# Optimization experiments

Hardware: AMD Instinct MI355X
Metric: run time of the kernel (lower is better)

The kernel has to match this reference:

```python
import jax, jax.numpy as jnp
import numpy as np

N = 100000          # nodes
E = 3200000         # edges per order (avg degree 32)
F_IN = 512          # num_features
HID = 128           # args.hidden
ORDER = 2
K = 10              # propagation hops
ALPHA = 0.1
C = 10              # num_classes


def setup_inputs() -> dict:
    key = jax.random.key(0)
    ks = jax.random.split(key, 10)
    x = jax.random.normal(ks[0], (N, F_IN), dtype=jnp.float32)
    edge_index1 = jax.random.randint(ks[1], (2, E), 0, N, dtype=jnp.int32)
    edge_weight1 = jax.random.uniform(ks[2], (E,), dtype=jnp.float32) / 32.0  # ~row-normalized
    edge_index2 = jax.random.randint(ks[3], (2, E), 0, N, dtype=jnp.int32)
    edge_weight2 = jax.random.uniform(ks[4], (E,), dtype=jnp.float32) / 32.0
    W_in = jax.random.normal(ks[5], (ORDER, F_IN, HID), dtype=jnp.float32) * 0.05
    b_in = jnp.zeros((ORDER, HID), dtype=jnp.float32)
    # GPR filter weights: fW[k] = alpha*(1-alpha)^k, fW[K] = (1-alpha)^K
    k_arr = np.arange(K + 1, dtype=np.float32)
    fw = ALPHA * (1.0 - ALPHA) ** k_arr
    fw[-1] = (1.0 - ALPHA) ** K
    fW = jnp.broadcast_to(jnp.asarray(fw), (ORDER, K + 1)).astype(jnp.float32)
    W_out = jax.random.normal(ks[6], (HID * ORDER, C), dtype=jnp.float32) * 0.05
    b_out = jnp.zeros((C,), dtype=jnp.float32)
    return {"x": x, "edge_index1": edge_index1, "edge_weight1": edge_weight1,
            "edge_index2": edge_index2, "edge_weight2": edge_weight2,
            "W_in": W_in, "b_in": b_in, "fW": fW, "W_out": W_out, "b_out": b_out}


def _spmm(edge_index, edge_weight, h, n):
    # y[row] += w * h[col]  (COO SpMM with add-aggregation)
    row, col = edge_index[0], edge_index[1]
    return jax.ops.segment_sum(edge_weight[:, None] * h[col], row, num_segments=n)


def reference(x, edge_index1, edge_weight1, edge_index2, edge_weight2,
              W_in, b_in, fW, W_out, b_out):
    n = x.shape[0]
    branches = [(edge_index1, edge_weight1), (edge_index2, edge_weight2)]
    outs = []
    for i, (ei, ew) in enumerate(branches):
        h = x @ W_in[i] + b_in[i]                 # [N, HID]  (dropout inactive in eval)
        hidden = h * fW[i, 0]
        for k in range(K):                        # K-hop GPR-weighted propagation
            h = _spmm(ei, ew, h, n)
            hidden = hidden + fW[i, k + 1] * h
        outs.append(hidden)
    z = jnp.concatenate(outs, axis=1) @ W_out + b_out   # [N, C]
    return jax.nn.log_softmax(z, axis=1)
```

## Files before the change

kernel.cpp:

```cpp
#include <hip/hip_runtime.h>

#define F_IN 512
#define HID 128
#define KHOPS 10
#define COUT 10

typedef unsigned int uint;
typedef unsigned short ushort;
typedef float f32x4 __attribute__((ext_vector_type(4)));
typedef short bf16x8 __attribute__((ext_vector_type(8)));
typedef int v16i __attribute__((ext_vector_type(16)));

__device__ __forceinline__ uint f2bf1(float f) {
    uint u = __float_as_uint(f);
    return (u + 0x7fffu + ((u >> 16) & 1u)) >> 16;
}
__device__ __forceinline__ uint packbf(float a, float b) {
    return f2bf1(a) | (f2bf1(b) << 16);
}
__device__ __forceinline__ float bflo(uint u) { return __uint_as_float(u << 16); }
__device__ __forceinline__ float bfhi(uint u) { return __uint_as_float(u & 0xffff0000u); }

__global__ __launch_bounds__(256) void wprep_kernel(
    const float* __restrict__ Win, ushort* __restrict__ Wsw)
{
    const int t = blockIdx.x * blockDim.x + threadIdx.x;
    if (t >= 2 * 16 * 8 * 64) return;
    const int l = t & 63;
    const int c = (t >> 6) & 7;
    const int s = (t >> 9) & 15;
    const int br = t >> 13;
    const int col = c * 16 + (l & 15);
    const int k0 = s * 32 + (l >> 4) * 8;
    const float* W = Win + (size_t)br * F_IN * HID;
    uint o0 = packbf(W[(size_t)(k0 + 0) * HID + col], W[(size_t)(k0 + 1) * HID + col]);
    uint o1 = packbf(W[(size_t)(k0 + 2) * HID + col], W[(size_t)(k0 + 3) * HID + col]);
    uint o2 = packbf(W[(size_t)(k0 + 4) * HID + col], W[(size_t)(k0 + 5) * HID + col]);
    uint o3 = packbf(W[(size_t)(k0 + 6) * HID + col], W[(size_t)(k0 + 7) * HID + col]);
    *(uint4*)(Wsw + (size_t)t * 8) = make_uint4(o0, o1, o2, o3);
}

__global__ __launch_bounds__(256) void gemm_mfma_kernel(
    const float* __restrict__ x, const ushort* __restrict__ Wsw,
    const float* __restrict__ bin, uint* __restrict__ h1, uint* __restrict__ h2, int n)
{
    const int br = blockIdx.y;
    const uint4* Wb = (const uint4*)(Wsw + (size_t)br * 16 * 8 * 64 * 8);
    const float* bias = bin + br * HID;
    uint* h = br ? h2 : h1;

    const int w = threadIdx.x >> 6;
    const int lane = threadIdx.x & 63;
    const int r16 = lane & 15;
    const int kg = lane >> 4;

    const int rowbase = blockIdx.x * 128 + w * 32;

    f32x4 acc[2][8];
#pragma unroll
    for (int f = 0; f < 2; ++f)
#pragma unroll
        for (int c = 0; c < 8; ++c) acc[f][c] = (f32x4)0.f;

    int rA0 = rowbase + r16;      if (rA0 > n - 1) rA0 = n - 1;
    int rA1 = rowbase + 16 + r16; if (rA1 > n - 1) rA1 = n - 1;
    const float* xp0 = x + (size_t)rA0 * F_IN + kg * 8;
    const float* xp1 = x + (size_t)rA1 * F_IN + kg * 8;

    for (int s = 0; s < 16; ++s) {
        const float4 a0lo = *(const float4*)(xp0 + s * 32);
        const float4 a0hi = *(const float4*)(xp0 + s * 32 + 4);
        const float4 a1lo = *(const float4*)(xp1 + s * 32);
        const float4 a1hi = *(const float4*)(xp1 + s * 32 + 4);
        union { uint4 u; bf16x8 v; } af0, af1;
        af0.u = make_uint4(packbf(a0lo.x, a0lo.y), packbf(a0lo.z, a0lo.w),
                           packbf(a0hi.x, a0hi.y), packbf(a0hi.z, a0hi.w));
        af1.u = make_uint4(packbf(a1lo.x, a1lo.y), packbf(a1lo.z, a1lo.w),
                           packbf(a1hi.x, a1hi.y), packbf(a1hi.z, a1hi.w));
        const uint4* wq = Wb + (size_t)(s * 8) * 64 + lane;
#pragma unroll
        for (int c = 0; c < 8; ++c) {
            union { uint4 u; bf16x8 v; } bfr;
            bfr.u = wq[c * 64];
            acc[0][c] = __builtin_amdgcn_mfma_f32_16x16x32_bf16(af0.v, bfr.v, acc[0][c], 0, 0, 0);
            acc[1][c] = __builtin_amdgcn_mfma_f32_16x16x32_bf16(af1.v, bfr.v, acc[1][c], 0, 0, 0);
        }
    }

    float bv[8];
#pragma unroll
    for (int c = 0; c < 8; ++c) bv[c] = bias[c * 16 + r16];

#pragma unroll
    for (int f = 0; f < 2; ++f)
#pragma unroll
        for (int c = 0; c < 8; ++c)
#pragma unroll
            for (int i = 0; i < 4; ++i) {
                const float v = acc[f][c][i] + bv[c];
                const float o = __shfl_xor(v, 1);
                const int row = rowbase + f * 16 + kg * 4 + i;
                if (!(lane & 1) && row < n)
                    h[(size_t)row * 64 + c * 8 + (r16 >> 1)] = packbf(v, o);
            }
}


__global__ void bhist_kernel(const int* __restrict__ r1, int E1,
                             const int* __restrict__ r2, int E2,
                             int* __restrict__ bcnt, int nb)
{
    extern __shared__ int sh[];
    const int br = blockIdx.y;
    const int* rows = br ? r2 : r1;
    const int E = br ? E2 : E1;
    int* bc = bcnt + (size_t)br * nb;
    for (int i = threadIdx.x; i < nb; i += blockDim.x) sh[i] = 0;
    __syncthreads();
    for (int i = blockIdx.x * blockDim.x + threadIdx.x; i < E; i += gridDim.x * blockDim.x)
        atomicAdd(&sh[rows[i] >> 6], 1);
    __syncthreads();
    for (int i = threadIdx.x; i < nb; i += blockDim.x)
        if (sh[i]) atomicAdd(&bc[i], sh[i]);
}

__global__ __launch_bounds__(256) void bscan_kernel(
    const int* __restrict__ bcnt, int* __restrict__ bbase, int* __restrict__ bcur,
    int* __restrict__ rowp1, int* __restrict__ rowp2,
    int nb, int n, int E1, int E2)
{
    __shared__ int ssum[256];
    const int br = blockIdx.y;
    const int* bc = bcnt + (size_t)br * nb;
    int* bb = bbase + (size_t)br * (nb + 1);
    int* cur = bcur + (size_t)br * nb;
    int* rowp = br ? rowp2 : rowp1;
    const int E = br ? E2 : E1;
    const int t = threadIdx.x;
    const int chunk = (nb + 255) / 256;
    const int start = t * chunk;
    const int end = (start + chunk < nb) ? start + chunk : nb;
    int sum = 0;
    for (int i = start; i < end; ++i) sum += bc[i];
    ssum[t] = sum;
    __syncthreads();
    if (t == 0) {
        int run = 0;
        for (int i = 0; i < 256; ++i) { int v = ssum[i]; ssum[i] = run; run += v; }
        bb[nb] = E;
        rowp[n] = E;
    }
    __syncthreads();
    int run = ssum[t];
    for (int i = start; i < end; ++i) {
        bb[i] = run; cur[i] = run; run += bc[i];
    }
}

#define SCAT_BLOCKS 256
__global__ __launch_bounds__(256) void bscat_kernel(
    const int* __restrict__ r1, const int* __restrict__ c1, const float* __restrict__ w1, int E1,
    const int* __restrict__ r2, const int* __restrict__ c2, const float* __restrict__ w2, int E2,
    int* __restrict__ bcur, int2* __restrict__ t1, int2* __restrict__ t2, int nb)
{
    extern __shared__ int sh[];
    int* lh = sh;
    int* lbase = sh + nb;
    const int br = blockIdx.y;
    const int* rows = br ? r2 : r1;
    const int* cols = br ? c2 : c1;
    const float* w  = br ? w2 : w1;
    const int E = br ? E2 : E1;
    int* cur = bcur + (size_t)br * nb;
    int2* tcw = br ? t2 : t1;
    const int t = threadIdx.x;

    for (int i = t; i < nb; i += 256) lh[i] = 0;
    __syncthreads();

    const int per = (E + SCAT_BLOCKS - 1) / SCAT_BLOCKS;
    const int c0 = blockIdx.x * per;
    const int cend = (c0 + per < E) ? c0 + per : E;

    for (int i = c0 + t; i < cend; i += 256)
        atomicAdd(&lh[rows[i] >> 6], 1);
    __syncthreads();
    for (int b = t; b < nb; b += 256) {
        int c = lh[b];
        lbase[b] = c ? atomicAdd(&cur[b], c) : 0;
        lh[b] = 0;
    }
    __syncthreads();
    for (int i = c0 + t; i < cend; i += 256) {
        int r = rows[i];
        int b = r >> 6;
        int p = atomicAdd(&lh[b], 1);
        uint lo = ((uint)cols[i] << 8) | (uint)(r & 63);
        tcw[lbase[b] + p] = make_int2((int)lo, __float_as_int(w[i]));
    }
}

__global__ __launch_bounds__(256) void bsort_kernel(
    const int* __restrict__ bbase,
    const int2* __restrict__ t1, const int2* __restrict__ t2,
    int* __restrict__ rowp1, int* __restrict__ rowp2,
    int2* __restrict__ cw1, int2* __restrict__ cw2, int nb, int n)
{
    __shared__ int cnt[64], soff[64], pos[64];
    const int br = blockIdx.y;
    const int* bb = bbase + (size_t)br * (nb + 1);
    const int2* tcw = br ? t2 : t1;
    int* rowp = br ? rowp2 : rowp1;
    int2* cw = br ? cw2 : cw1;
    const int b = blockIdx.x;
    const int t = threadIdx.x;
    const int base = bb[b];
    const int m = bb[b + 1] - base;
    if (t < 64) cnt[t] = 0;
    __syncthreads();
    for (int i = t; i < m; i += 256) atomicAdd(&cnt[(uint)tcw[base + i].x & 63], 1);
    __syncthreads();
    if (t == 0) {
        int run = 0;
#pragma unroll
        for (int r = 0; r < 64; ++r) { soff[r] = run; run += cnt[r]; }
    }
    __syncthreads();
    if (t < 64) {
        pos[t] = soff[t];
        int g = b * 64 + t;
        if (g < n) rowp[g] = base + soff[t];
    }
    __syncthreads();
    for (int i = t; i < m; i += 256) {
        int2 e = tcw[base + i];
        int r = (uint)e.x & 63;
        int p = atomicAdd(&pos[r], 1);
        cw[base + p] = make_int2((int)((uint)e.x & 0xFFFFFF00u), e.y);
    }
}

struct BrArgs {
    const int* rowp;
    const int2* cw;
    const uint* hin;
    uint* hout;
    const float* Wo;
};

__global__ __launch_bounds__(256) void spmm2_kernel(
    BrArgs A, BrArgs B, const float* __restrict__ fW, int k,
    float* __restrict__ z2, int storeH, int n)
{
    const int bid = blockIdx.x;
    const int br = bid & 1;
    const int wid = (bid >> 1) * 4 + (threadIdx.x >> 6);
    if (wid >= n) return;
    const int*   rowp = br ? B.rowp : A.rowp;
    const int2*  cw   = br ? B.cw   : A.cw;
    const uint*  hin  = br ? B.hin  : A.hin;
    uint*        hout = br ? B.hout : A.hout;
    const float* Wo   = br ? B.Wo   : A.Wo;
    const int lane = threadIdx.x & 63;
    const uint laneB = (uint)lane * 4u;
    const char* hbase = (const char*)hin;

    float w0[COUT], w1[COUT];
    const float* wp = Wo + (size_t)(lane * 2) * COUT;
#pragma unroll
    for (int c = 0; c < COUT; ++c) { w0[c] = wp[c]; w1[c] = wp[COUT + c]; }

    int s = rowp[wid];
    int e = rowp[wid + 1];
    s = __builtin_amdgcn_readfirstlane(s);
    e = __builtin_amdgcn_readfirstlane(e);

    float2 acc = make_float2(0.f, 0.f);
    int i = s;

    while (e - i >= 16) {
        v16i e0v, e1v;
        asm volatile("s_load_dwordx16 %0, %2, 0x0\n\t"
                     "s_load_dwordx16 %1, %2, 0x40\n\t"
                     "s_waitcnt lgkmcnt(0)"
                     : "=s"(e0v), "=s"(e1v) : "s"(cw + i));
#pragma unroll
        for (int j = 0; j < 8; ++j) {
            const uint boff = (uint)e0v[2 * j];
            const float q = __int_as_float(e0v[2 * j + 1]);
            const uint g = *(const uint*)(hbase + (size_t)boff + laneB);
            acc.x = fmaf(q, bflo(g), acc.x);
            acc.y = fmaf(q, bfhi(g), acc.y);
        }
#pragma unroll
        for (int j = 0; j < 8; ++j) {
            const uint boff = (uint)e1v[2 * j];
            const float q = __int_as_float(e1v[2 * j + 1]);
            const uint g = *(const uint*)(hbase + (size_t)boff + laneB);
            acc.x = fmaf(q, bflo(g), acc.x);
            acc.y = fmaf(q, bfhi(g), acc.y);
        }
        i += 16;
    }
    const int rem = e - i;
    if (rem > 0) {
        v16i e0v, e1v;
        asm volatile("s_load_dwordx16 %0, %2, 0x0\n\t"
                     "s_load_dwordx16 %1, %2, 0x40\n\t"
                     "s_waitcnt lgkmcnt(0)"
                     : "=s"(e0v), "=s"(e1v) : "s"(cw + i));
#pragma unroll
        for (int j = 0; j < 16; ++j) {
            uint boff = (uint)((j < 8) ? e0v[2 * j] : e1v[2 * (j - 8)]);
            float q = __int_as_float((j < 8) ? e0v[2 * j + 1] : e1v[2 * (j - 8) + 1]);
            if (j >= rem) { boff = 0u; q = 0.f; }
            const uint g = *(const uint*)(hbase + (size_t)boff + laneB);
            acc.x = fmaf(q, bflo(g), acc.x);
            acc.y = fmaf(q, bfhi(g), acc.y);
        }
    }

    if (storeH)
        hout[(size_t)wid * 64 + lane] = packbf(acc.x, acc.y);

    const float fw = fW[br * (KHOPS + 1) + k + 1];
    float zadd = 0.f;
#pragma unroll
    for (int c = 0; c < COUT; ++c) {
        float pp = fmaf(acc.x, w0[c], acc.y * w1[c]);
#pragma unroll
        for (int off = 32; off; off >>= 1) pp += __shfl_xor(pp, off);
        if (lane == c) zadd = pp;
    }
    if (lane < COUT) {
        const size_t o = (size_t)wid * (2 * COUT) + br * COUT + lane;
        z2[o] += fw * zadd;
    }
}

__global__ __launch_bounds__(256) void zacc2_kernel(
    const uint* __restrict__ h1, const uint* __restrict__ h2,
    const float* __restrict__ Wout, const float* __restrict__ fW,
    float* __restrict__ z2, int n)
{
    const int wid = (blockIdx.x * blockDim.x + threadIdx.x) >> 6;
    if (wid >= n) return;
    const int lane = threadIdx.x & 63;
    const uint u1 = h1[(size_t)wid * 64 + lane];
    const uint u2 = h2[(size_t)wid * 64 + lane];
    const float a1 = bflo(u1), b1v = bfhi(u1);
    const float a2 = bflo(u2), b2v = bfhi(u2);
    const float* wp1 = Wout + (size_t)(lane * 2) * COUT;
    const float* wp2 = Wout + (size_t)HID * COUT + (size_t)(lane * 2) * COUT;
    float zv1 = 0.f, zv2 = 0.f;
#pragma unroll
    for (int c = 0; c < COUT; ++c) {
        float p1 = fmaf(a1, wp1[c], b1v * wp1[COUT + c]);
        float p2 = fmaf(a2, wp2[c], b2v * wp2[COUT + c]);
#pragma unroll
        for (int off = 32; off; off >>= 1) { p1 += __shfl_xor(p1, off); p2 += __shfl_xor(p2, off); }
        if (lane == c) { zv1 = p1; zv2 = p2; }
    }
    if (lane < COUT) {
        z2[(size_t)wid * (2 * COUT) + lane]        = fW[0] * zv1;
        z2[(size_t)wid * (2 * COUT) + COUT + lane] = fW[KHOPS + 1] * zv2;
    }
}

__global__ void logsm_kernel(const float* __restrict__ z2, const float* __restrict__ bout,
                             float* __restrict__ out, int n)
{
    const int r = blockIdx.x * blockDim.x + threadIdx.x;
    if (r >= n) return;
    float v[COUT];
    float m = -1e30f;
#pragma unroll
    for (int c = 0; c < COUT; ++c) {
        v[c] = z2[(size_t)r * (2 * COUT) + c] + z2[(size_t)r * (2 * COUT) + COUT + c] + bout[c];
        m = fmaxf(m, v[c]);
    }
    float s = 0.f;
#pragma unroll
    for (int c = 0; c < COUT; ++c) s += expf(v[c] - m);
    const float l = logf(s) + m;
#pragma unroll
    for (int c = 0; c < COUT; ++c) out[(size_t)r * COUT + c] = v[c] - l;
}

extern "C" void kernel_launch(void* const* d_in, const int* in_sizes, int n_in,
                              void* d_out, int out_size, void* d_ws, size_t ws_size,
                              hipStream_t stream)
{
    const float* x    = (const float*)d_in[0];
    const int*   ei1  = (const int*)d_in[1];
    const float* ew1  = (const float*)d_in[2];
    const int*   ei2  = (const int*)d_in[3];
    const float* ew2  = (const float*)d_in[4];
    const float* Win  = (const float*)d_in[5];
    const float* bin  = (const float*)d_in[6];
    const float* fW   = (const float*)d_in[7];
    const float* Wout = (const float*)d_in[8];
    const float* bout = (const float*)d_in[9];
    const int n  = in_sizes[0] / F_IN;
    const int E1 = in_sizes[2];
    const int E2 = in_sizes[4];
    const int Emax = E1 > E2 ? E1 : E2;
    const int nb = (n + 63) / 64;
    float* zout = (float*)d_out;

    char* p = (char*)d_ws;
    auto alloc = [&](size_t bytes) { char* r = p; p += (bytes + 255) & ~(size_t)255; return r; };
    char* regA = alloc((size_t)4 * n * 64 * 4);
    uint* h1A = (uint*)regA;
    uint* h1B = (uint*)(regA + (size_t)n * 64 * 4);
    uint* h2A = (uint*)(regA + (size_t)2 * n * 64 * 4);
    uint* h2B = (uint*)(regA + (size_t)3 * n * 64 * 4);
    int2* tcw1 = (int2*)regA;
    int2* tcw2 = (int2*)(regA + (size_t)Emax * 8);
    int2* cw1  = (int2*)alloc((size_t)Emax * 8 + 128);
    int2* cw2  = (int2*)alloc((size_t)Emax * 8 + 128);
    int*  rowp1 = (int*)alloc((size_t)(n + 1) * 4);
    int*  rowp2 = (int*)alloc((size_t)(n + 1) * 4);
    float* z2  = (float*)alloc((size_t)n * 2 * COUT * 4);
    int*  bcnt  = (int*)alloc((size_t)2 * nb * 4);
    int*  bbase = (int*)alloc((size_t)2 * (nb + 1) * 4);
    int*  bcur  = (int*)alloc((size_t)2 * nb * 4);
    ushort* Wsw = (ushort*)alloc((size_t)2 * 16 * 8 * 64 * 8 * 2);

    const int rowBlocks = (n + 3) / 4;

    hipLaunchKernelGGL(wprep_kernel, dim3(64), dim3(256), 0, stream, Win, Wsw);

    hipMemsetAsync(bcnt, 0, (size_t)2 * nb * 4, stream);
    hipLaunchKernelGGL(bhist_kernel, dim3(256, 2), dim3(256), nb * 4, stream,
                       ei1, E1, ei2, E2, bcnt, nb);
    hipLaunchKernelGGL(bscan_kernel, dim3(1, 2), dim3(256), 0, stream,
                       bcnt, bbase, bcur, rowp1, rowp2, nb, n, E1, E2);
    hipLaunchKernelGGL(bscat_kernel, dim3(SCAT_BLOCKS, 2), dim3(256), 2 * nb * 4, stream,
                       ei1, ei1 + E1, ew1, E1, ei2, ei2 + E2, ew2, E2,
                       bcur, tcw1, tcw2, nb);
    hipLaunchKernelGGL(bsort_kernel, dim3(nb, 2), dim3(256), 0, stream,
                       bbase, tcw1, tcw2, rowp1, rowp2, cw1, cw2, nb, n);

    hipLaunchKernelGGL(gemm_mfma_kernel, dim3((n + 127) / 128, 2), dim3(256), 0, stream,
                       x, Wsw, bin, h1A, h2A, n);

    hipLaunchKernelGGL(zacc2_kernel, dim3(rowBlocks), dim3(256), 0, stream,
                       h1A, h2A, Wout, fW, z2, n);

    uint* cur1 = h1A; uint* nxt1 = h1B;
    uint* cur2 = h2A; uint* nxt2 = h2B;
    for (int k = 0; k < KHOPS; ++k) {
        const int storeH = (k < KHOPS - 1) ? 1 : 0;
        BrArgs A { rowp1, cw1, cur1, nxt1, Wout };
        BrArgs B { rowp2, cw2, cur2, nxt2, Wout + (size_t)HID * COUT };
        hipLaunchKernelGGL(spmm2_kernel, dim3(rowBlocks * 2), dim3(256), 0, stream,
                           A, B, fW, k, z2, storeH, n);
        uint* t1 = cur1; cur1 = nxt1; nxt1 = t1;
        uint* t2 = cur2; cur2 = nxt2; nxt2 = t2;
    }

    hipLaunchKernelGGL(logsm_kernel, dim3((n + 255) / 256), dim3(256), 0, stream,
                       z2, bout, zout, n);
}
```

Measured before the change: 3.038 ms.

## Split wave into four edge groups with 16-byte row gathers in SpMM

The SpMM kernel now splits each 64-lane wavefront into four groups of 16 lanes. Each group handles a different edge, and each lane gathers a 16-byte uint4 chunk (8 bf16 values) of the neighbour row. This replaces the old scheme of one edge at a time across the full wave with scalar-loaded edge batches. Partial sums are combined with cross-group shuffles, and the output projection is split across groups, three classes per group. This cuts the per-edge instruction count and uses wider memory transactions, at the cost of per-lane edge loads and extra shuffle reductions.

```diff
diff --git a/kernel.cpp b/kernel.cpp
--- a/kernel.cpp
+++ b/kernel.cpp
@@ -9,7 +9,6 @@
 typedef unsigned short ushort;
 typedef float f32x4 __attribute__((ext_vector_type(4)));
 typedef short bf16x8 __attribute__((ext_vector_type(8)));
-typedef int v16i __attribute__((ext_vector_type(16)));
 
 __device__ __forceinline__ uint f2bf1(float f) {
     uint u = __float_as_uint(f);
@@ -262,79 +261,83 @@
     uint*        hout = br ? B.hout : A.hout;
     const float* Wo   = br ? B.Wo   : A.Wo;
     const int lane = threadIdx.x & 63;
-    const uint laneB = (uint)lane * 4u;
+    const int g   = lane >> 4;
+    const int sub = lane & 15;
+    const uint subB = (uint)sub * 16u;
     const char* hbase = (const char*)hin;
 
-    float w0[COUT], w1[COUT];
-    const float* wp = Wo + (size_t)(lane * 2) * COUT;
-#pragma unroll
-    for (int c = 0; c < COUT; ++c) { w0[c] = wp[c]; w1[c] = wp[COUT + c]; }
-
-    int s = rowp[wid];
-    int e = rowp[wid + 1];
-    s = __builtin_amdgcn_readfirstlane(s);
-    e = __builtin_amdgcn_readfirstlane(e);
-
-    float2 acc = make_float2(0.f, 0.f);
+    float wv[8][3];
+#pragma unroll
+    for (int j = 0; j < 8; ++j)
+#pragma unroll
+        for (int s2 = 0; s2 < 3; ++s2) {
+            const int c = g * 3 + s2;
+            wv[j][s2] = (c < COUT) ? Wo[(size_t)(sub * 8 + j) * COUT + c] : 0.f;
+        }
+
+    const int s = rowp[wid];
+    const int e = rowp[wid + 1];
+
+    float a[8];
+#pragma unroll
+    for (int j = 0; j < 8; ++j) a[j] = 0.f;
+
     int i = s;
-
-    while (e - i >= 16) {
-        v16i e0v, e1v;
-        asm volatile("s_load_dwordx16 %0, %2, 0x0\n\t"
-                     "s_load_dwordx16 %1, %2, 0x40\n\t"
-                     "s_waitcnt lgkmcnt(0)"
-                     : "=s"(e0v), "=s"(e1v) : "s"(cw + i));
-#pragma unroll
-        for (int j = 0; j < 8; ++j) {
-            const uint boff = (uint)e0v[2 * j];
-            const float q = __int_as_float(e0v[2 * j + 1]);
-            const uint g = *(const uint*)(hbase + (size_t)boff + laneB);
-            acc.x = fmaf(q, bflo(g), acc.x);
-            acc.y = fmaf(q, bfhi(g), acc.y);
-        }
-#pragma unroll
-        for (int j = 0; j < 8; ++j) {
-            const uint boff = (uint)e1v[2 * j];
-            const float q = __int_as_float(e1v[2 * j + 1]);
-            const uint g = *(const uint*)(hbase + (size_t)boff + laneB);
-            acc.x = fmaf(q, bflo(g), acc.x);
-            acc.y = fmaf(q, bfhi(g), acc.y);
-        }
-        i += 16;
+    for (; i + 4 <= e; i += 4) {
+        const int2 my = cw[i + g];
+        const float q = __int_as_float(my.y);
+        const uint4 gv = *(const uint4*)(hbase + ((uint)my.x + subB));
+        a[0] = fmaf(q, bflo(gv.x), a[0]); a[1] = fmaf(q, bfhi(gv.x), a[1]);
+        a[2] = fmaf(q, bflo(gv.y), a[2]); a[3] = fmaf(q, bfhi(gv.y), a[3]);
+        a[4] = fmaf(q, bflo(gv.z), a[4]); a[5] = fmaf(q, bfhi(gv.z), a[5]);
+        a[6] = fmaf(q, bflo(gv.w), a[6]); a[7] = fmaf(q, bfhi(gv.w), a[7]);
     }
     const int rem = e - i;
     if (rem > 0) {
-        v16i e0v, e1v;
-        asm volatile("s_load_dwordx16 %0, %2, 0x0\n\t"
-                     "s_load_dwordx16 %1, %2, 0x40\n\t"
-                     "s_waitcnt lgkmcnt(0)"
-                     : "=s"(e0v), "=s"(e1v) : "s"(cw + i));
-#pragma unroll
-        for (int j = 0; j < 16; ++j) {
-            uint boff = (uint)((j < 8) ? e0v[2 * j] : e1v[2 * (j - 8)]);
-            float q = __int_as_float((j < 8) ? e0v[2 * j + 1] : e1v[2 * (j - 8) + 1]);
-            if (j >= rem) { boff = 0u; q = 0.f; }
-            const uint g = *(const uint*)(hbase + (size_t)boff + laneB);
-            acc.x = fmaf(q, bflo(g), acc.x);
-            acc.y = fmaf(q, bfhi(g), acc.y);
-        }
-    }
-
-    if (storeH)
-        hout[(size_t)wid * 64 + lane] = packbf(acc.x, acc.y);
-
-    const float fw = fW[br * (KHOPS + 1) + k + 1];
-    float zadd = 0.f;
-#pragma unroll
-    for (int c = 0; c < COUT; ++c) {
-        float pp = fmaf(acc.x, w0[c], acc.y * w1[c]);
-#pragma unroll
-        for (int off = 32; off; off >>= 1) pp += __shfl_xor(pp, off);
-        if (lane == c) zadd = pp;
-    }
-    if (lane < COUT) {
-        const size_t o = (size_t)wid * (2 * COUT) + br * COUT + lane;
-        z2[o] += fw * zadd;
+        const int2 my = cw[i + g];
+        const bool ok = g < rem;
+        const float q = ok ? __int_as_float(my.y) : 0.f;
+        const uint boff = ok ? (uint)my.x : 0u;
+        const uint4 gv = *(const uint4*)(hbase + (boff + subB));
+        a[0] = fmaf(q, bflo(gv.x), a[0]); a[1] = fmaf(q, bfhi(gv.x), a[1]);
+        a[2] = fmaf(q, bflo(gv.y), a[2]); a[3] = fmaf(q, bfhi(gv.y), a[3]);
+        a[4] = fmaf(q, bflo(gv.z), a[4]); a[5] = fmaf(q, bfhi(gv.z), a[5]);
+        a[6] = fmaf(q, bflo(gv.w), a[6]); a[7] = fmaf(q, bfhi(gv.w), a[7]);
+    }
+
+#pragma unroll
+    for (int j = 0; j < 8; ++j) {
+        a[j] += __shfl_xor(a[j], 16);
+        a[j] += __shfl_xor(a[j], 32);
+    }
+
+    if (storeH && lane < 16) {
+        uint4 o;
+        o.x = packbf(a[0], a[1]);
+        o.y = packbf(a[2], a[3]);
+        o.z = packbf(a[4], a[5]);
+        o.w = packbf(a[6], a[7]);
+        *(uint4*)((char*)hout + (size_t)wid * 256 + subB) = o;
+    }
+
+    float zr0 = 0.f, zr1 = 0.f, zr2 = 0.f;
+#pragma unroll
+    for (int j = 0; j < 8; ++j) {
+        zr0 = fmaf(a[j], wv[j][0], zr0);
+        zr1 = fmaf(a[j], wv[j][1], zr1);
+        zr2 = fmaf(a[j], wv[j][2], zr2);
+    }
+#pragma unroll
+    for (int off = 8; off; off >>= 1) {
+        zr0 += __shfl_xor(zr0, off);
+        zr1 += __shfl_xor(zr1, off);
+        zr2 += __shfl_xor(zr2, off);
+    }
+    const int c = g * 3 + sub;
+    if (sub < 3 && c < COUT) {
+        const float zsel = (sub == 0) ? zr0 : (sub == 1) ? zr1 : zr2;
+        const float fw = fW[br * (KHOPS + 1) + k + 1];
+        z2[(size_t)wid * (2 * COUT) + br * COUT + c] += fw * zsel;
     }
 }
 
```

New measurement: 6.185 ms. 104% more time.
